# Kernel tuning notes

Hardware: AMD Instinct MI355X
Metric: run time of the kernel (lower is better)

The kernel has to match this reference:

```python
import jax, jax.numpy as jnp
import numpy as np

S = 2              # scaling_factor
RBF_RADIUS = 2
RADIUS = S * RBF_RADIUS   # high-res pixel radius = 4
WIN = 3                   # 3x3 candidate window -> K = 9 = MAX_NEIGHBOURS
K = WIN * WIN


def setup_inputs() -> dict:
    key = jax.random.key(0)
    k0, k1, k2, k3, k4, k5, k6 = jax.random.split(key, 7)
    A, n, c, h, w = 4, 4, 3, 256, 256
    sh, sw = S * h, S * w
    alts = jax.random.normal(k0, (A, n, c, h, w), jnp.float32)
    # sub-pixel motion offsets in low-res units; clipped so every output pixel
    # keeps at least one valid neighbor inside the RBF radius
    offsets = jnp.clip(0.5 * jax.random.normal(k1, (A, n, 2, h, w), jnp.float32), -1.0, 1.0)
    qs = jax.random.uniform(k2, (A, n, h, w), jnp.float32, minval=0.1, maxval=1.0)
    o11 = jax.random.uniform(k3, (n, sh, sw), jnp.float32, minval=0.5, maxval=2.0)
    o22 = jax.random.uniform(k4, (n, sh, sw), jnp.float32, minval=0.5, maxval=2.0)
    o12 = jax.random.uniform(k5, (n, sh, sw), jnp.float32, minval=-0.2, maxval=0.2)
    o21 = jax.random.uniform(k6, (n, sh, sw), jnp.float32, minval=-0.2, maxval=0.2)
    return {"alts": alts, "offsets": offsets, "qs": qs,
            "o11": o11, "o12": o12, "o21": o21, "o22": o22}


def reference(alts, offsets, qs, o11, o12, o21, o22):
    A, n, c, h, w = alts.shape
    sh, sw = S * h, S * w
    yy = jnp.arange(sh)
    xx = jnp.arange(sw)
    y0 = yy // S                      # base low-res row for each output row
    x0 = xx // S
    d = jnp.arange(WIN) - WIN // 2
    di, dj = jnp.meshgrid(d, d, indexing="ij")
    di, dj = di.ravel(), dj.ravel()   # (K,)
    rn_raw = y0[:, None, None] + di[None, None, :]   # (sh,1,K)
    cn_raw = x0[None, :, None] + dj[None, None, :]   # (1,sw,K)
    inb = ((rn_raw >= 0) & (rn_raw < h) & (cn_raw >= 0) & (cn_raw < w))  # (sh,sw,K)
    rn = jnp.clip(rn_raw, 0, h - 1)
    cn = jnp.clip(cn_raw, 0, w - 1)
    yy_f = yy.astype(jnp.float32)[None, :, None, None]   # (1,sh,1,1)
    xx_f = xx.astype(jnp.float32)[None, None, :, None]   # (1,1,sw,1)
    rn_f = rn.astype(jnp.float32)
    cn_f = cn.astype(jnp.float32)

    x_out = 0.0
    weights = 0.0
    for a in range(A):   # small fixed number of alternate frames
        off_r = offsets[a][:, 0][:, rn, cn]              # (n,sh,sw,K)
        off_c = offsets[a][:, 1][:, rn, cn]
        pos_r = rn_f * S + off_r * S                     # shifted sample positions (high-res)
        pos_c = cn_f * S + off_c * S
        # neighbor validity: in-bounds grid cell and within RBF radius
        a_neigh = (inb & (jnp.abs(pos_r - yy_f) <= RADIUS)
                       & (jnp.abs(pos_c - xx_f) <= RADIUS)).astype(jnp.float32)
        dy = (pos_r - yy_f) / S                          # displacement in low-res units
        dx = (pos_c - xx_f) / S
        rbf_dist = (dx * dx * o11[..., None] + dx * dy * o12[..., None]
                    + dy * dx * o21[..., None] + dy * dy * o22[..., None])
        rbf_w = jnp.exp(-0.5 * jnp.clip(rbf_dist, 0.0, 20.0))
        q_w = qs[a][:, rn, cn]                           # (n,sh,sw,K)
        wgt = rbf_w * q_w * a_neigh
        weights = weights + jnp.sum(wgt, axis=3)         # (n,sh,sw)
        alt_neigh = alts[a][:, :, rn, cn]                # (n,c,sh,sw,K)
        x_out = x_out + jnp.einsum("ncyxk,nyxk->ncyx", alt_neigh, wgt)
    return x_out / weights[:, None, :, :]
```

## Files before the change

### kernel.cpp

```cpp
#include <hip/hip_runtime.h>


#define AF      4
#define NB      4
#define CH      3
#define H       256
#define W       256
#define SH      512
#define SW      512
#define HW      (H*W)
#define SHW     (SH*SW)
#define RADIUS  4.0f
#define MSCALE  0.18033688011112042f

__global__ __launch_bounds__(256) void superresolve_kernel(
    const float* __restrict__ alts,
    const float* __restrict__ offsets,
    const float* __restrict__ qs,
    const float* __restrict__ o11,
    const float* __restrict__ o12,
    const float* __restrict__ o21,
    const float* __restrict__ o22,
    float* __restrict__ out)
{
    __shared__ float red[3 * 64 * 17];

    const int tid  = threadIdx.x;
    const int wv   = tid >> 6;
    const int lane = tid & 63;

    const int bid = blockIdx.x;
    const int swz = (bid & 7) * 512 + (bid >> 3);
    const int x0 = ((swz & 3) << 6) + lane;
    const int y0 = __builtin_amdgcn_readfirstlane((swz >> 2) & (H - 1));
    const int nn = __builtin_amdgcn_readfirstlane(swz >> 10);
    const int a  = __builtin_amdgcn_readfirstlane(wv);

    const bool bL = (x0 > 0);
    const bool bR = (x0 < W - 1);
    const int  xL = bL ? x0 - 1 : 0;
    const int  xR = bR ? x0 + 1 : W - 1;
    const int  iL = y0 * W + xL;
    const int  iC = y0 * W + x0;
    const int  iR = y0 * W + xR;
    const float f2xL = (float)(2 * xL);
    const float f2xC = (float)(2 * x0);
    const float f2xR = (float)(2 * xR);
    const float xf0  = f2xC;
    const float yf0  = (float)(2 * y0);

    const int obase = (nn * SH + 2 * y0) * SW + 2 * x0;
    const float2 v11a = *(const float2*)(o11 + obase);
    const float2 v11b = *(const float2*)(o11 + obase + SW);
    const float2 v12a = *(const float2*)(o12 + obase);
    const float2 v12b = *(const float2*)(o12 + obase + SW);
    const float2 v21a = *(const float2*)(o21 + obase);
    const float2 v21b = *(const float2*)(o21 + obase + SW);
    const float2 v22a = *(const float2*)(o22 + obase);
    const float2 v22b = *(const float2*)(o22 + obase + SW);

    float m11s[2][2], m12s[2][2], m22s[2][2];
    m11s[0][0] = MSCALE * v11a.x;  m11s[0][1] = MSCALE * v11a.y;
    m11s[1][0] = MSCALE * v11b.x;  m11s[1][1] = MSCALE * v11b.y;
    m12s[0][0] = MSCALE * (v12a.x + v21a.x);  m12s[0][1] = MSCALE * (v12a.y + v21a.y);
    m12s[1][0] = MSCALE * (v12b.x + v21b.x);  m12s[1][1] = MSCALE * (v12b.y + v21b.y);
    m22s[0][0] = MSCALE * v22a.x;  m22s[0][1] = MSCALE * v22a.y;
    m22s[1][0] = MSCALE * v22b.x;  m22s[1][1] = MSCALE * v22b.y;

    float sumw[2][2] = {{0.f,0.f},{0.f,0.f}};
    float acc0[2][2] = {{0.f,0.f},{0.f,0.f}};
    float acc1[2][2] = {{0.f,0.f},{0.f,0.f}};
    float acc2[2][2] = {{0.f,0.f},{0.f,0.f}};

#define COLK(or_, oc_, q_, a0_, a1_, a2_, f2x_, IS_L, NEED_VY)                \
    {                                                                         \
        const float posr = fmaf(or_, 2.0f, rowf);                             \
        const float dy0v = posr - yf0;                                        \
        const float dy1v = dy0v - 1.0f;                                       \
        const float posc = fmaf(oc_, 2.0f, f2x_);                             \
        const float dx0v = posc - xf0;                                        \
        const float dx1v = dx0v - 1.0f;                                       \
        const bool vx1 = !(IS_L) || (dx1v >= -RADIUS);                        \
        const bool vyb = !(NEED_VY) || (dy1v >= -RADIUS);                     \
        _Pragma("unroll")                                                     \
        for (int sy = 0; sy < 2; ++sy) {                                      \
            const float dyv = sy ? dy1v : dy0v;                               \
            const float dy2 = dyv * dyv;                                      \
            _Pragma("unroll")                                                 \
            for (int sx = 0; sx < 2; ++sx) {                                  \
                const float dxv = sx ? dx1v : dx0v;                           \
                const float u = fmaf(dyv, m12s[sy][sx], dxv * m11s[sy][sx]);  \
                const float d = fmaf(dxv, u, dy2 * m22s[sy][sx]);             \
                float w = __builtin_amdgcn_exp2f(-d) * (q_);                  \
                if (IS_L && sx == 1)    w = vx1 ? w : 0.0f;                   \
                if (NEED_VY && sy == 1) w = vyb ? w : 0.0f;                   \
                sumw[sy][sx] += w;                                            \
                acc0[sy][sx] = fmaf(w, a0_, acc0[sy][sx]);                    \
                acc1[sy][sx] = fmaf(w, a1_, acc1[sy][sx]);                    \
                acc2[sy][sx] = fmaf(w, a2_, acc2[sy][sx]);                    \
            }                                                                 \
        }                                                                     \
    }

    {
        const float* offbR = offsets + (size_t)(a * NB + nn) * 2 * HW;
        const float* offbC = offbR + HW;
        const float* qb    = qs   + (size_t)(a * NB + nn) * HW;
        const float* ab0   = alts + (size_t)(a * NB + nn) * CH * HW;
        const float* ab1   = ab0 + HW;
        const float* ab2   = ab0 + 2 * HW;

        #pragma unroll
        for (int dr = 0; dr < 3; ++dr) {
            if (dr == 0 && y0 == 0) continue;
            if (dr == 2 && y0 == H - 1) continue;
            const int ro = (dr - 1) * W;
            const float* pR = offbR + ro;
            const float* pC = offbC + ro;
            const float* pQ = qb + ro;
            const float* p0 = ab0 + ro;
            const float* p1 = ab1 + ro;
            const float* p2 = ab2 + ro;
            const float rowf = (float)(2 * (y0 + dr - 1));

            const float orL = pR[iL], orC = pR[iC], orR = pR[iR];
            const float ocL = pC[iL], ocC = pC[iC], ocR = pC[iR];
            const float qL  = pQ[iL], qC  = pQ[iC], qR  = pQ[iR];
            const float aL0 = p0[iL], aC0 = p0[iC], aR0 = p0[iR];
            const float aL1 = p1[iL], aC1 = p1[iC], aR1 = p1[iR];
            const float aL2 = p2[iL], aC2 = p2[iC], aR2 = p2[iR];

            const float qLm = bL ? qL : 0.0f;
            const float qRm = bR ? qR : 0.0f;

            const bool needvy = (dr == 0);
            COLK(orL, ocL, qLm, aL0, aL1, aL2, f2xL, true,  needvy)
            COLK(orC, ocC, qC,  aC0, aC1, aC2, f2xC, false, needvy)
            COLK(orR, ocR, qRm, aR0, aR1, aR2, f2xR, false, needvy)
        }
    }
#undef COLK

    if (wv != 0) {
        float* r = &red[((wv - 1) * 64 + lane) * 17];
        #pragma unroll
        for (int sy = 0; sy < 2; ++sy)
            #pragma unroll
            for (int sx = 0; sx < 2; ++sx) {
                const int s = sy * 2 + sx;
                r[s]      = sumw[sy][sx];
                r[4 + s]  = acc0[sy][sx];
                r[8 + s]  = acc1[sy][sx];
                r[12 + s] = acc2[sy][sx];
            }
    }
    __syncthreads();
    if (wv == 0) {
        #pragma unroll
        for (int w = 0; w < 3; ++w) {
            const float* r = &red[(w * 64 + lane) * 17];
            #pragma unroll
            for (int sy = 0; sy < 2; ++sy)
                #pragma unroll
                for (int sx = 0; sx < 2; ++sx) {
                    const int s = sy * 2 + sx;
                    sumw[sy][sx] += r[s];
                    acc0[sy][sx] += r[4 + s];
                    acc1[sy][sx] += r[8 + s];
                    acc2[sy][sx] += r[12 + s];
                }
        }
        const size_t ob = (size_t)(nn * CH) * SHW + (size_t)(2 * y0) * SW + 2 * x0;
        #pragma unroll
        for (int sy = 0; sy < 2; ++sy) {
            const float i0 = 1.0f / sumw[sy][0];
            const float i1 = 1.0f / sumw[sy][1];
            *(float2*)(out + ob + (size_t)sy * SW) =
                make_float2(acc0[sy][0] * i0, acc0[sy][1] * i1);
            *(float2*)(out + ob + (size_t)sy * SW + SHW) =
                make_float2(acc1[sy][0] * i0, acc1[sy][1] * i1);
            *(float2*)(out + ob + (size_t)sy * SW + 2 * SHW) =
                make_float2(acc2[sy][0] * i0, acc2[sy][1] * i1);
        }
    }
}

extern "C" void kernel_launch(void* const* d_in, const int* in_sizes, int n_in,
                              void* d_out, int out_size, void* d_ws, size_t ws_size,
                              hipStream_t stream) {
    const float* alts    = (const float*)d_in[0];
    const float* offsets = (const float*)d_in[1];
    const float* qs      = (const float*)d_in[2];
    const float* o11     = (const float*)d_in[3];
    const float* o12     = (const float*)d_in[4];
    const float* o21     = (const float*)d_in[5];
    const float* o22     = (const float*)d_in[6];
    float* out = (float*)d_out;

    const int total_threads = NB * H * W * 4;
    const int block = 256;
    const int grid  = total_threads / block;
    superresolve_kernel<<<grid, block, 0, stream>>>(alts, offsets, qs,
                                                    o11, o12, o21, o22, out);
}
```

Measured before the change: 23.85 us.

## Split work per wave by output sub-row and frame pair instead of per frame

Each wave now handles two alternate frames for one output sub-row (sy) rather than one frame for all four sub-pixels. The change cuts per-thread accumulators and the o-matrix loads, shrinks the shared-memory reduction from four waves' partials to two, and lets two waves write outputs instead of one. It also sets launch bounds to 8 blocks per CU to target higher occupancy. In exchange, each wave reloads the low-res neighbour data for both of its frames, and the same neighbours are loaded by the two sy-waves, so global and cache load traffic doubles.

After: 24.04 us. No clear change (+0.8%).

```diff
diff --git a/kernel.cpp b/kernel.cpp
--- a/kernel.cpp
+++ b/kernel.cpp
@@ -13,7 +13,7 @@
 #define RADIUS  4.0f
 #define MSCALE  0.18033688011112042f
 
-__global__ __launch_bounds__(256) void superresolve_kernel(
+__global__ __launch_bounds__(256, 8) void superresolve_kernel(
     const float* __restrict__ alts,
     const float* __restrict__ offsets,
     const float* __restrict__ qs,
@@ -23,18 +23,21 @@
     const float* __restrict__ o22,
     float* __restrict__ out)
 {
-    __shared__ float red[3 * 64 * 17];
+    __shared__ float red[2 * 64 * 9];
 
     const int tid  = threadIdx.x;
     const int wv   = tid >> 6;
     const int lane = tid & 63;
+    const int fpair = wv >> 1;
+    const int syh   = wv & 1;
 
     const int bid = blockIdx.x;
     const int swz = (bid & 7) * 512 + (bid >> 3);
     const int x0 = ((swz & 3) << 6) + lane;
-    const int y0 = __builtin_amdgcn_readfirstlane((swz >> 2) & (H - 1));
-    const int nn = __builtin_amdgcn_readfirstlane(swz >> 10);
-    const int a  = __builtin_amdgcn_readfirstlane(wv);
+    const int y0  = __builtin_amdgcn_readfirstlane((swz >> 2) & (H - 1));
+    const int nn  = __builtin_amdgcn_readfirstlane(swz >> 10);
+    const int af0 = __builtin_amdgcn_readfirstlane(fpair << 1);
+    const int sy  = __builtin_amdgcn_readfirstlane(syh);
 
     const bool bL = (x0 > 0);
     const bool bR = (x0 < W - 1);
@@ -47,62 +50,52 @@
     const float f2xC = (float)(2 * x0);
     const float f2xR = (float)(2 * xR);
     const float xf0  = f2xC;
-    const float yf0  = (float)(2 * y0);
+    const float yfS  = (float)(2 * y0 + sy);
 
-    const int obase = (nn * SH + 2 * y0) * SW + 2 * x0;
-    const float2 v11a = *(const float2*)(o11 + obase);
-    const float2 v11b = *(const float2*)(o11 + obase + SW);
-    const float2 v12a = *(const float2*)(o12 + obase);
-    const float2 v12b = *(const float2*)(o12 + obase + SW);
-    const float2 v21a = *(const float2*)(o21 + obase);
-    const float2 v21b = *(const float2*)(o21 + obase + SW);
-    const float2 v22a = *(const float2*)(o22 + obase);
-    const float2 v22b = *(const float2*)(o22 + obase + SW);
+    const int obase = (nn * SH + 2 * y0 + sy) * SW + 2 * x0;
+    const float2 v11 = *(const float2*)(o11 + obase);
+    const float2 v12 = *(const float2*)(o12 + obase);
+    const float2 v21 = *(const float2*)(o21 + obase);
+    const float2 v22 = *(const float2*)(o22 + obase);
 
-    float m11s[2][2], m12s[2][2], m22s[2][2];
-    m11s[0][0] = MSCALE * v11a.x;  m11s[0][1] = MSCALE * v11a.y;
-    m11s[1][0] = MSCALE * v11b.x;  m11s[1][1] = MSCALE * v11b.y;
-    m12s[0][0] = MSCALE * (v12a.x + v21a.x);  m12s[0][1] = MSCALE * (v12a.y + v21a.y);
-    m12s[1][0] = MSCALE * (v12b.x + v21b.x);  m12s[1][1] = MSCALE * (v12b.y + v21b.y);
-    m22s[0][0] = MSCALE * v22a.x;  m22s[0][1] = MSCALE * v22a.y;
-    m22s[1][0] = MSCALE * v22b.x;  m22s[1][1] = MSCALE * v22b.y;
+    const float m11x = MSCALE * v11.x, m11y = MSCALE * v11.y;
+    const float m12x = MSCALE * (v12.x + v21.x), m12y = MSCALE * (v12.y + v21.y);
+    const float m22x = MSCALE * v22.x, m22y = MSCALE * v22.y;
 
-    float sumw[2][2] = {{0.f,0.f},{0.f,0.f}};
-    float acc0[2][2] = {{0.f,0.f},{0.f,0.f}};
-    float acc1[2][2] = {{0.f,0.f},{0.f,0.f}};
-    float acc2[2][2] = {{0.f,0.f},{0.f,0.f}};
+    float sumw0 = 0.f, sumw1 = 0.f;
+    float a00 = 0.f, a01 = 0.f;
+    float a10 = 0.f, a11 = 0.f;
+    float a20 = 0.f, a21 = 0.f;
 
-#define COLK(or_, oc_, q_, a0_, a1_, a2_, f2x_, IS_L, NEED_VY)                \
+#define COLK(or_, oc_, q_, a0_, a1_, a2_, f2x_, IS_L, DR0)                    \
     {                                                                         \
         const float posr = fmaf(or_, 2.0f, rowf);                             \
-        const float dy0v = posr - yf0;                                        \
-        const float dy1v = dy0v - 1.0f;                                       \
+        const float dyv  = posr - yfS;                                        \
         const float posc = fmaf(oc_, 2.0f, f2x_);                             \
         const float dx0v = posc - xf0;                                        \
         const float dx1v = dx0v - 1.0f;                                       \
-        const bool vx1 = !(IS_L) || (dx1v >= -RADIUS);                        \
-        const bool vyb = !(NEED_VY) || (dy1v >= -RADIUS);                     \
-        _Pragma("unroll")                                                     \
-        for (int sy = 0; sy < 2; ++sy) {                                      \
-            const float dyv = sy ? dy1v : dy0v;                               \
-            const float dy2 = dyv * dyv;                                      \
-            _Pragma("unroll")                                                 \
-            for (int sx = 0; sx < 2; ++sx) {                                  \
-                const float dxv = sx ? dx1v : dx0v;                           \
-                const float u = fmaf(dyv, m12s[sy][sx], dxv * m11s[sy][sx]);  \
-                const float d = fmaf(dxv, u, dy2 * m22s[sy][sx]);             \
-                float w = __builtin_amdgcn_exp2f(-d) * (q_);                  \
-                if (IS_L && sx == 1)    w = vx1 ? w : 0.0f;                   \
-                if (NEED_VY && sy == 1) w = vyb ? w : 0.0f;                   \
-                sumw[sy][sx] += w;                                            \
-                acc0[sy][sx] = fmaf(w, a0_, acc0[sy][sx]);                    \
-                acc1[sy][sx] = fmaf(w, a1_, acc1[sy][sx]);                    \
-                acc2[sy][sx] = fmaf(w, a2_, acc2[sy][sx]);                    \
-            }                                                                 \
+        const float dy2  = dyv * dyv;                                         \
+        const float u0 = fmaf(dyv, m12x, dx0v * m11x);                        \
+        const float d0 = fmaf(dx0v, u0, dy2 * m22x);                          \
+        const float u1 = fmaf(dyv, m12y, dx1v * m11y);                        \
+        const float d1 = fmaf(dx1v, u1, dy2 * m22y);                          \
+        float w0 = __builtin_amdgcn_exp2f(-d0) * (q_);                        \
+        float w1 = __builtin_amdgcn_exp2f(-d1) * (q_);                        \
+        if (IS_L) w1 = (dx1v >= -RADIUS) ? w1 : 0.0f;                         \
+        if (DR0 && sy) {                                                      \
+            const bool vy = (dyv >= -RADIUS);                                 \
+            w0 = vy ? w0 : 0.0f;                                              \
+            w1 = vy ? w1 : 0.0f;                                              \
         }                                                                     \
+        sumw0 += w0;            sumw1 += w1;                                  \
+        a00 = fmaf(w0, a0_, a00); a01 = fmaf(w1, a0_, a01);                   \
+        a10 = fmaf(w0, a1_, a10); a11 = fmaf(w1, a1_, a11);                   \
+        a20 = fmaf(w0, a2_, a20); a21 = fmaf(w1, a2_, a21);                   \
     }
 
-    {
+    #pragma unroll
+    for (int ai = 0; ai < 2; ++ai) {
+        const int a = af0 + ai;
         const float* offbR = offsets + (size_t)(a * NB + nn) * 2 * HW;
         const float* offbC = offbR + HW;
         const float* qb    = qs   + (size_t)(a * NB + nn) * HW;
@@ -133,55 +126,36 @@
             const float qLm = bL ? qL : 0.0f;
             const float qRm = bR ? qR : 0.0f;
 
-            const bool needvy = (dr == 0);
-            COLK(orL, ocL, qLm, aL0, aL1, aL2, f2xL, true,  needvy)
-            COLK(orC, ocC, qC,  aC0, aC1, aC2, f2xC, false, needvy)
-            COLK(orR, ocR, qRm, aR0, aR1, aR2, f2xR, false, needvy)
+            const bool dr0 = (dr == 0);
+            COLK(orL, ocL, qLm, aL0, aL1, aL2, f2xL, true,  dr0)
+            COLK(orC, ocC, qC,  aC0, aC1, aC2, f2xC, false, dr0)
+            COLK(orR, ocR, qRm, aR0, aR1, aR2, f2xR, false, dr0)
         }
     }
 #undef COLK
 
-    if (wv != 0) {
-        float* r = &red[((wv - 1) * 64 + lane) * 17];
-        #pragma unroll
-        for (int sy = 0; sy < 2; ++sy)
-            #pragma unroll
-            for (int sx = 0; sx < 2; ++sx) {
-                const int s = sy * 2 + sx;
-                r[s]      = sumw[sy][sx];
-                r[4 + s]  = acc0[sy][sx];
-                r[8 + s]  = acc1[sy][sx];
-                r[12 + s] = acc2[sy][sx];
-            }
+    if (fpair == 1) {
+        float* r = &red[(syh * 64 + lane) * 9];
+        r[0] = sumw0; r[1] = sumw1;
+        r[2] = a00;   r[3] = a01;
+        r[4] = a10;   r[5] = a11;
+        r[6] = a20;   r[7] = a21;
     }
     __syncthreads();
-    if (wv == 0) {
-        #pragma unroll
-        for (int w = 0; w < 3; ++w) {
-            const float* r = &red[(w * 64 + lane) * 17];
-            #pragma unroll
-            for (int sy = 0; sy < 2; ++sy)
-                #pragma unroll
-                for (int sx = 0; sx < 2; ++sx) {
-                    const int s = sy * 2 + sx;
-                    sumw[sy][sx] += r[s];
-                    acc0[sy][sx] += r[4 + s];
-                    acc1[sy][sx] += r[8 + s];
-                    acc2[sy][sx] += r[12 + s];
-                }
-        }
-        const size_t ob = (size_t)(nn * CH) * SHW + (size_t)(2 * y0) * SW + 2 * x0;
-        #pragma unroll
-        for (int sy = 0; sy < 2; ++sy) {
-            const float i0 = 1.0f / sumw[sy][0];
-            const float i1 = 1.0f / sumw[sy][1];
-            *(float2*)(out + ob + (size_t)sy * SW) =
-                make_float2(acc0[sy][0] * i0, acc0[sy][1] * i1);
-            *(float2*)(out + ob + (size_t)sy * SW + SHW) =
-                make_float2(acc1[sy][0] * i0, acc1[sy][1] * i1);
-            *(float2*)(out + ob + (size_t)sy * SW + 2 * SHW) =
-                make_float2(acc2[sy][0] * i0, acc2[sy][1] * i1);
-        }
+    if (fpair == 0) {
+        const float* r = &red[(syh * 64 + lane) * 9];
+        sumw0 += r[0]; sumw1 += r[1];
+        a00 += r[2];   a01 += r[3];
+        a10 += r[4];   a11 += r[5];
+        a20 += r[6];   a21 += r[7];
+
+        const float i0 = 1.0f / sumw0;
+        const float i1 = 1.0f / sumw1;
+        const size_t ob = (size_t)(nn * CH) * SHW
+                        + (size_t)(2 * y0 + sy) * SW + 2 * x0;
+        *(float2*)(out + ob)           = make_float2(a00 * i0, a01 * i1);
+        *(float2*)(out + ob + SHW)     = make_float2(a10 * i0, a11 * i1);
+        *(float2*)(out + ob + 2*SHW)   = make_float2(a20 * i0, a21 * i1);
     }
 }
 
```
